# Optimization experiments

Measured on AMD Instinct MI355X. Metric: run time of the kernel, lower is better.

The kernel has to match this reference:

```python
import jax, jax.numpy as jnp
import numpy as np

B, H, S, D = 2, 16, 2048, 64

def setup_inputs() -> dict:
    key = jax.random.key(0)
    kq, kk, kv = jax.random.split(key, 3)
    Q = jax.random.normal(kq, (B, H, S, D), dtype=jnp.float32)
    K = jax.random.normal(kk, (B, H, S, D), dtype=jnp.float32)
    V = jax.random.normal(kv, (B, H, S, D), dtype=jnp.float32)
    return {"Q": Q, "K": K, "V": V}

def reference(Q, K, V):
    # scores: [B, H, S, S]
    scale = 1.0 / jnp.sqrt(jnp.asarray(Q.shape[-1], Q.dtype))
    scores = jnp.einsum('bhqd,bhkd->bhqk', Q, K) * scale
    probs = jax.nn.softmax(scores, axis=-1)
    out = jnp.einsum('bhqk,bhkd->bhqd', probs, V)
    return out
```

## Files before the change

### kernel.cpp

```cpp
#include <hip/hip_runtime.h>
#include <hip/hip_bf16.h>


#define Bn 2
#define Hn 16
#define Sn 2048
#define Dn 64
#define KP 72
#define OP 68

typedef __attribute__((ext_vector_type(8)))  short s16x8;
typedef __attribute__((ext_vector_type(16))) float f32x16;

__device__ __forceinline__ float fast_exp2(float x) {
#if __has_builtin(__builtin_amdgcn_exp2f)
    return __builtin_amdgcn_exp2f(x);
#else
    return exp2f(x);
#endif
}
__device__ __forceinline__ unsigned short f2bf(float f) {
    unsigned u = __float_as_uint(f);
    return (unsigned short)((u + 0x7fffu + ((u >> 16) & 1u)) >> 16);
}
__device__ __forceinline__ unsigned pack2bf(float lo, float hi) {
    return (unsigned)f2bf(lo) | ((unsigned)f2bf(hi) << 16);
}
__device__ __forceinline__ unsigned packtrunc(float lo, float hi) {
#if __has_builtin(__builtin_amdgcn_perm)
    return __builtin_amdgcn_perm(__float_as_uint(hi), __float_as_uint(lo),
                                 0x07060302u);
#else
    return (__float_as_uint(lo) >> 16) | (__float_as_uint(hi) & 0xffff0000u);
#endif
}
__device__ __forceinline__ s16x8 lds_frag(const unsigned short* p) {
    uint4 u = *(const uint4*)p;
    return __builtin_bit_cast(s16x8, u);
}
__device__ __forceinline__ s16x8 reg_frag(uint4 u) {
    return __builtin_bit_cast(s16x8, u);
}

__global__ __launch_bounds__(256)
void cast_kv2(const float* __restrict__ K, const float* __restrict__ V,
              unsigned short* __restrict__ Kb, unsigned short* __restrict__ Vt) {
    __shared__ unsigned short TK[64 * 72];
    __shared__ unsigned short TV[64 * 72];
    const int tid = threadIdx.x;
    const int bh  = blockIdx.x >> 5;
    const int kt  = blockIdx.x & 31;
    const int r = tid >> 2, cc = (tid & 3) * 16;

    const size_t rowbase = ((size_t)bh * Sn + (size_t)kt * 64 + r) * Dn + cc;
    {
        const float* ks = K + rowbase;
        #pragma unroll
        for (int i = 0; i < 2; ++i) {
            float4 f0 = *(const float4*)(ks + 8 * i);
            float4 f1 = *(const float4*)(ks + 8 * i + 4);
            uint4 w;
            w.x = pack2bf(f0.x, f0.y); w.y = pack2bf(f0.z, f0.w);
            w.z = pack2bf(f1.x, f1.y); w.w = pack2bf(f1.z, f1.w);
            *(uint4*)(TK + r * 72 + cc + 8 * i) = w;
        }
    }
    {
        const float* vs = V + rowbase;
        #pragma unroll
        for (int i = 0; i < 4; ++i) {
            float4 f = *(const float4*)(vs + 4 * i);
            const int d0 = cc + 4 * i;
            TV[(d0 + 0) * 72 + r] = f2bf(f.x);
            TV[(d0 + 1) * 72 + r] = f2bf(f.y);
            TV[(d0 + 2) * 72 + r] = f2bf(f.z);
            TV[(d0 + 3) * 72 + r] = f2bf(f.w);
        }
    }
    __syncthreads();
    unsigned short* kd = Kb + ((size_t)(bh * 32 + kt) * 8) * 512;
    unsigned short* vd = Vt + ((size_t)(bh * 32 + kt) * 8) * 512;
    #pragma unroll
    for (int i = 0; i < 2; ++i) {
        const int u = i * 256 + tid;
        const int c = u >> 6, lane = u & 63;
        const int l31 = lane & 31, hf = lane >> 5;
        const int sub = c >> 2, ks = c & 3;
        const int off = (sub * 32 + l31) * 72 + ks * 16 + hf * 8;
        *(uint4*)(kd + c * 512 + lane * 8) = *(const uint4*)(TK + off);
        *(uint4*)(vd + c * 512 + lane * 8) = *(const uint4*)(TV + off);
    }
}

__global__ __launch_bounds__(128, 2)
void attn_fwd_mfma4(const float* __restrict__ Q,
                    const unsigned short* __restrict__ Kb,
                    const unsigned short* __restrict__ Vt,
                    float* __restrict__ O) {
    __shared__ __align__(16) char smem[18432];
    unsigned short* PT = (unsigned short*)smem;
    float* ob = (float*)smem;
    float* lb = ob + 64 * OP;

    const int tid  = threadIdx.x;
    const int wave = tid >> 6;
    const int lane = tid & 63;
    const int l31  = lane & 31;
    const int half = lane >> 5;

    const int bh = blockIdx.x & 31;
    const int q0 = (blockIdx.x >> 5) * 64;

    const float* Qb = Q + ((size_t)bh * Sn + q0) * Dn;
    const float FCT = 0.18033688011112042f;

    s16x8 qf[2][4];
    #pragma unroll
    for (int s = 0; s < 2; ++s) {
        const float* qp = Qb + (size_t)(s * 32 + l31) * Dn;
        #pragma unroll
        for (int ks = 0; ks < 4; ++ks) {
            const int d0 = ks * 16 + half * 8;
            float4 f0 = *(const float4*)(qp + d0);
            float4 f1 = *(const float4*)(qp + d0 + 4);
            uint4 u;
            u.x = pack2bf(f0.x * FCT, f0.y * FCT);
            u.y = pack2bf(f0.z * FCT, f0.w * FCT);
            u.z = pack2bf(f1.x * FCT, f1.y * FCT);
            u.w = pack2bf(f1.z * FCT, f1.w * FCT);
            qf[s][ks] = __builtin_bit_cast(s16x8, u);
        }
    }

    f32x16 acc00, acc01, acc10, acc11;
    #pragma unroll
    for (int r = 0; r < 16; ++r) { acc00[r]=0.f; acc01[r]=0.f; acc10[r]=0.f; acc11[r]=0.f; }
    float l0 = 0.f, l1 = 0.f;

    const unsigned short* kbase =
        Kb + ((size_t)(bh * 32 + wave * 16) * 8) * 512 + (size_t)lane * 8;
    const unsigned short* vbase =
        Vt + ((size_t)(bh * 32 + wave * 16) * 8) * 512 + (size_t)lane * 8;

    unsigned short* ptw0 = PT + ((size_t)wave * 64 + l31) * KP;
    unsigned short* ptw1 = ptw0 + 32 * KP;

    uint4 kbuf[2][8], vv[8];
    #pragma unroll
    for (int c = 0; c < 8; ++c)
        kbuf[0][c] = *(const uint4*)(kbase + c * 512);

    #pragma unroll
    for (int t = 0; t < 16; ++t) {
        uint4* CUR = kbuf[t & 1];
        uint4* NXT = kbuf[(t + 1) & 1];
        #pragma unroll
        for (int c = 0; c < 8; ++c)
            vv[c] = *(const uint4*)(vbase + (size_t)(t * 8 + c) * 512);
        const int tk = (t < 15 ? t + 1 : 15);
        #pragma unroll
        for (int c = 0; c < 8; ++c)
            NXT[c] = *(const uint4*)(kbase + (size_t)(tk * 8 + c) * 512);

        #pragma unroll
        for (int s = 0; s < 2; ++s) {
            f32x16 c0, c1;
            #pragma unroll
            for (int r = 0; r < 16; ++r) { c0[r] = 0.f; c1[r] = 0.f; }
            #pragma unroll
            for (int ks = 0; ks < 4; ++ks) {
                c0 = __builtin_amdgcn_mfma_f32_32x32x16_bf16(reg_frag(CUR[ks]),     qf[s][ks], c0, 0, 0, 0);
                c1 = __builtin_amdgcn_mfma_f32_32x32x16_bf16(reg_frag(CUR[4 + ks]), qf[s][ks], c1, 0, 0, 0);
            }
            #pragma unroll
            for (int r = 0; r < 16; ++r) {
                c0[r] = fast_exp2(c0[r]);
                c1[r] = fast_exp2(c1[r]);
            }
            float a0 = 0.f, a1 = 0.f, a2 = 0.f, a3 = 0.f;
            #pragma unroll
            for (int r = 0; r < 16; r += 4) {
                a0 += c0[r] + c1[r];
                a1 += c0[r + 1] + c1[r + 1];
                a2 += c0[r + 2] + c1[r + 2];
                a3 += c0[r + 3] + c1[r + 3];
            }
            if (s == 0) l0 += (a0 + a1) + (a2 + a3);
            else        l1 += (a0 + a1) + (a2 + a3);

            unsigned short* ptw = s ? ptw1 : ptw0;
            #pragma unroll
            for (int g = 0; g < 4; ++g) {
                uint2 w0, w1;
                w0.x = packtrunc(c0[4 * g + 0], c0[4 * g + 1]);
                w0.y = packtrunc(c0[4 * g + 2], c0[4 * g + 3]);
                w1.x = packtrunc(c1[4 * g + 0], c1[4 * g + 1]);
                w1.y = packtrunc(c1[4 * g + 2], c1[4 * g + 3]);
                *(uint2*)(ptw + 8 * g + 4 * half)      = w0;
                *(uint2*)(ptw + 8 * g + 4 * half + 32) = w1;
            }
        }

        #pragma unroll
        for (int ks = 0; ks < 4; ++ks) {
            const int off = ks * 16 + half * 8;
            s16x8 pf0 = lds_frag(ptw0 + off);
            s16x8 pf1 = lds_frag(ptw1 + off);
            s16x8 va  = reg_frag(vv[ks]);
            s16x8 vb  = reg_frag(vv[4 + ks]);
            acc00 = __builtin_amdgcn_mfma_f32_32x32x16_bf16(va, pf0, acc00, 0, 0, 0);
            acc01 = __builtin_amdgcn_mfma_f32_32x32x16_bf16(vb, pf0, acc01, 0, 0, 0);
            acc10 = __builtin_amdgcn_mfma_f32_32x32x16_bf16(va, pf1, acc10, 0, 0, 0);
            acc11 = __builtin_amdgcn_mfma_f32_32x32x16_bf16(vb, pf1, acc11, 0, 0, 0);
        }
    }

    l0 += __shfl_xor(l0, 32, 64);
    l1 += __shfl_xor(l1, 32, 64);

    __syncthreads();
    if (wave == 0) {
        #pragma unroll
        for (int g = 0; g < 4; ++g) {
            const int d0 = 8 * g + 4 * half;
            float4 f;
            f.x = acc00[4*g+0]; f.y = acc00[4*g+1]; f.z = acc00[4*g+2]; f.w = acc00[4*g+3];
            *(float4*)(ob + l31 * OP + d0) = f;
            f.x = acc01[4*g+0]; f.y = acc01[4*g+1]; f.z = acc01[4*g+2]; f.w = acc01[4*g+3];
            *(float4*)(ob + l31 * OP + d0 + 32) = f;
            f.x = acc10[4*g+0]; f.y = acc10[4*g+1]; f.z = acc10[4*g+2]; f.w = acc10[4*g+3];
            *(float4*)(ob + (32 + l31) * OP + d0) = f;
            f.x = acc11[4*g+0]; f.y = acc11[4*g+1]; f.z = acc11[4*g+2]; f.w = acc11[4*g+3];
            *(float4*)(ob + (32 + l31) * OP + d0 + 32) = f;
        }
        if (half == 0) { lb[l31] = l0; lb[32 + l31] = l1; }
    }
    __syncthreads();
    if (wave == 1) {
        const float i0 = 1.0f / (l0 + lb[l31]);
        const float i1 = 1.0f / (l1 + lb[32 + l31]);
        #pragma unroll
        for (int g = 0; g < 4; ++g) {
            const int d0 = 8 * g + 4 * half;
            float4 f;
            float* p;
            p = ob + l31 * OP + d0;            f = *(float4*)p;
            f.x = (f.x + acc00[4*g+0]) * i0; f.y = (f.y + acc00[4*g+1]) * i0;
            f.z = (f.z + acc00[4*g+2]) * i0; f.w = (f.w + acc00[4*g+3]) * i0;
            *(float4*)p = f;
            p = ob + l31 * OP + d0 + 32;       f = *(float4*)p;
            f.x = (f.x + acc01[4*g+0]) * i0; f.y = (f.y + acc01[4*g+1]) * i0;
            f.z = (f.z + acc01[4*g+2]) * i0; f.w = (f.w + acc01[4*g+3]) * i0;
            *(float4*)p = f;
            p = ob + (32 + l31) * OP + d0;     f = *(float4*)p;
            f.x = (f.x + acc10[4*g+0]) * i1; f.y = (f.y + acc10[4*g+1]) * i1;
            f.z = (f.z + acc10[4*g+2]) * i1; f.w = (f.w + acc10[4*g+3]) * i1;
            *(float4*)p = f;
            p = ob + (32 + l31) * OP + d0 + 32; f = *(float4*)p;
            f.x = (f.x + acc11[4*g+0]) * i1; f.y = (f.y + acc11[4*g+1]) * i1;
            f.z = (f.z + acc11[4*g+2]) * i1; f.w = (f.w + acc11[4*g+3]) * i1;
            *(float4*)p = f;
        }
    }
    __syncthreads();
    float* op = O + ((size_t)bh * Sn + q0) * Dn;
    #pragma unroll
    for (int it = 0; it < 8; ++it) {
        const int idx = it * 128 + tid;
        const int r = idx >> 4, c4 = (idx & 15) * 4;
        *(float4*)(op + r * Dn + c4) = *(float4*)(ob + r * OP + c4);
    }
}

extern "C" void kernel_launch(void* const* d_in, const int* in_sizes, int n_in,
                              void* d_out, int out_size, void* d_ws, size_t ws_size,
                              hipStream_t stream) {
    const float* Q = (const float*)d_in[0];
    const float* K = (const float*)d_in[1];
    const float* V = (const float*)d_in[2];
    float* O = (float*)d_out;

    const size_t elems = (size_t)Bn * Hn * Sn * Dn;
    unsigned short* Kb = (unsigned short*)d_ws;
    unsigned short* Vt = Kb + elems;

    cast_kv2<<<dim3(Bn * Hn * (Sn / 64)), dim3(256), 0, stream>>>(K, V, Kb, Vt);
    attn_fwd_mfma4<<<dim3(Bn * Hn * (Sn / 64)), dim3(128), 0, stream>>>(Q, Kb, Vt, O);
}
```

Measured before the change: 131.5 us.

## Split query rows across four waves per block and drop K double-buffering

The attention kernel now launches 256 threads per block. Each of four waves handles 32 query rows against one half of the keys, where before two waves each handled 64 query rows. This halves per-wave accumulator and register state and doubles the waves available to hide latency. The register double-buffered K prefetch and full unroll of the key-tile loop are removed in favour of a non-unrolled loop with loads issued just before use. Each wave now loads the same K/V tiles as one other wave, so global and L2 traffic per block doubles. Latency hiding now depends on occupancy rather than explicit prefetch.

```diff
diff --git a/kernel.cpp b/kernel.cpp
--- a/kernel.cpp
+++ b/kernel.cpp
@@ -92,8 +92,8 @@
     }
 }
 
-__global__ __launch_bounds__(128, 2)
-void attn_fwd_mfma4(const float* __restrict__ Q,
+__global__ __launch_bounds__(256, 4)
+void attn_fwd_mfma5(const float* __restrict__ Q,
                     const unsigned short* __restrict__ Kb,
                     const unsigned short* __restrict__ Vt,
                     float* __restrict__ O) {
@@ -107,17 +107,17 @@
     const int lane = tid & 63;
     const int l31  = lane & 31;
     const int half = lane >> 5;
+    const int qg   = wave & 1;
+    const int kh   = wave >> 1;
 
     const int bh = blockIdx.x & 31;
     const int q0 = (blockIdx.x >> 5) * 64;
 
-    const float* Qb = Q + ((size_t)bh * Sn + q0) * Dn;
     const float FCT = 0.18033688011112042f;
 
-    s16x8 qf[2][4];
-    #pragma unroll
-    for (int s = 0; s < 2; ++s) {
-        const float* qp = Qb + (size_t)(s * 32 + l31) * Dn;
+    s16x8 qf[4];
+    {
+        const float* qp = Q + ((size_t)bh * Sn + q0 + qg * 32 + l31) * Dn;
         #pragma unroll
         for (int ks = 0; ks < 4; ++ks) {
             const int d0 = ks * 16 + half * 8;
@@ -128,145 +128,116 @@
             u.y = pack2bf(f0.z * FCT, f0.w * FCT);
             u.z = pack2bf(f1.x * FCT, f1.y * FCT);
             u.w = pack2bf(f1.z * FCT, f1.w * FCT);
-            qf[s][ks] = __builtin_bit_cast(s16x8, u);
-        }
-    }
-
-    f32x16 acc00, acc01, acc10, acc11;
+            qf[ks] = __builtin_bit_cast(s16x8, u);
+        }
+    }
+
+    f32x16 acc0, acc1;
     #pragma unroll
-    for (int r = 0; r < 16; ++r) { acc00[r]=0.f; acc01[r]=0.f; acc10[r]=0.f; acc11[r]=0.f; }
-    float l0 = 0.f, l1 = 0.f;
+    for (int r = 0; r < 16; ++r) { acc0[r] = 0.f; acc1[r] = 0.f; }
+    float l = 0.f;
 
     const unsigned short* kbase =
-        Kb + ((size_t)(bh * 32 + wave * 16) * 8) * 512 + (size_t)lane * 8;
+        Kb + ((size_t)(bh * 32 + kh * 16) * 8) * 512 + (size_t)lane * 8;
     const unsigned short* vbase =
-        Vt + ((size_t)(bh * 32 + wave * 16) * 8) * 512 + (size_t)lane * 8;
-
-    unsigned short* ptw0 = PT + ((size_t)wave * 64 + l31) * KP;
-    unsigned short* ptw1 = ptw0 + 32 * KP;
-
-    uint4 kbuf[2][8], vv[8];
-    #pragma unroll
-    for (int c = 0; c < 8; ++c)
-        kbuf[0][c] = *(const uint4*)(kbase + c * 512);
-
-    #pragma unroll
+        Vt + ((size_t)(bh * 32 + kh * 16) * 8) * 512 + (size_t)lane * 8;
+
+    unsigned short* ptw = PT + ((size_t)wave * 32 + l31) * KP;
+
+    #pragma unroll 1
     for (int t = 0; t < 16; ++t) {
-        uint4* CUR = kbuf[t & 1];
-        uint4* NXT = kbuf[(t + 1) & 1];
+        uint4 kk[8];
+        #pragma unroll
+        for (int c = 0; c < 8; ++c)
+            kk[c] = *(const uint4*)(kbase + (size_t)(t * 8 + c) * 512);
+
+        f32x16 c0, c1;
+        #pragma unroll
+        for (int r = 0; r < 16; ++r) { c0[r] = 0.f; c1[r] = 0.f; }
+        #pragma unroll
+        for (int ks = 0; ks < 4; ++ks) {
+            c0 = __builtin_amdgcn_mfma_f32_32x32x16_bf16(reg_frag(kk[ks]),     qf[ks], c0, 0, 0, 0);
+            c1 = __builtin_amdgcn_mfma_f32_32x32x16_bf16(reg_frag(kk[4 + ks]), qf[ks], c1, 0, 0, 0);
+        }
+
+        uint4 vv[8];
         #pragma unroll
         for (int c = 0; c < 8; ++c)
             vv[c] = *(const uint4*)(vbase + (size_t)(t * 8 + c) * 512);
-        const int tk = (t < 15 ? t + 1 : 15);
-        #pragma unroll
-        for (int c = 0; c < 8; ++c)
-            NXT[c] = *(const uint4*)(kbase + (size_t)(tk * 8 + c) * 512);
-
-        #pragma unroll
-        for (int s = 0; s < 2; ++s) {
-            f32x16 c0, c1;
-            #pragma unroll
-            for (int r = 0; r < 16; ++r) { c0[r] = 0.f; c1[r] = 0.f; }
-            #pragma unroll
-            for (int ks = 0; ks < 4; ++ks) {
-                c0 = __builtin_amdgcn_mfma_f32_32x32x16_bf16(reg_frag(CUR[ks]),     qf[s][ks], c0, 0, 0, 0);
-                c1 = __builtin_amdgcn_mfma_f32_32x32x16_bf16(reg_frag(CUR[4 + ks]), qf[s][ks], c1, 0, 0, 0);
-            }
-            #pragma unroll
-            for (int r = 0; r < 16; ++r) {
-                c0[r] = fast_exp2(c0[r]);
-                c1[r] = fast_exp2(c1[r]);
-            }
-            float a0 = 0.f, a1 = 0.f, a2 = 0.f, a3 = 0.f;
-            #pragma unroll
-            for (int r = 0; r < 16; r += 4) {
-                a0 += c0[r] + c1[r];
-                a1 += c0[r + 1] + c1[r + 1];
-                a2 += c0[r + 2] + c1[r + 2];
-                a3 += c0[r + 3] + c1[r + 3];
-            }
-            if (s == 0) l0 += (a0 + a1) + (a2 + a3);
-            else        l1 += (a0 + a1) + (a2 + a3);
-
-            unsigned short* ptw = s ? ptw1 : ptw0;
-            #pragma unroll
-            for (int g = 0; g < 4; ++g) {
-                uint2 w0, w1;
-                w0.x = packtrunc(c0[4 * g + 0], c0[4 * g + 1]);
-                w0.y = packtrunc(c0[4 * g + 2], c0[4 * g + 3]);
-                w1.x = packtrunc(c1[4 * g + 0], c1[4 * g + 1]);
-                w1.y = packtrunc(c1[4 * g + 2], c1[4 * g + 3]);
-                *(uint2*)(ptw + 8 * g + 4 * half)      = w0;
-                *(uint2*)(ptw + 8 * g + 4 * half + 32) = w1;
-            }
+
+        #pragma unroll
+        for (int r = 0; r < 16; ++r) {
+            c0[r] = fast_exp2(c0[r]);
+            c1[r] = fast_exp2(c1[r]);
+        }
+        float a0 = 0.f, a1 = 0.f, a2 = 0.f, a3 = 0.f;
+        #pragma unroll
+        for (int r = 0; r < 16; r += 4) {
+            a0 += c0[r]     + c1[r];
+            a1 += c0[r + 1] + c1[r + 1];
+            a2 += c0[r + 2] + c1[r + 2];
+            a3 += c0[r + 3] + c1[r + 3];
+        }
+        l += (a0 + a1) + (a2 + a3);
+
+        #pragma unroll
+        for (int g = 0; g < 4; ++g) {
+            uint2 w0, w1;
+            w0.x = packtrunc(c0[4 * g + 0], c0[4 * g + 1]);
+            w0.y = packtrunc(c0[4 * g + 2], c0[4 * g + 3]);
+            w1.x = packtrunc(c1[4 * g + 0], c1[4 * g + 1]);
+            w1.y = packtrunc(c1[4 * g + 2], c1[4 * g + 3]);
+            *(uint2*)(ptw + 8 * g + 4 * half)      = w0;
+            *(uint2*)(ptw + 8 * g + 4 * half + 32) = w1;
         }
 
         #pragma unroll
         for (int ks = 0; ks < 4; ++ks) {
-            const int off = ks * 16 + half * 8;
-            s16x8 pf0 = lds_frag(ptw0 + off);
-            s16x8 pf1 = lds_frag(ptw1 + off);
-            s16x8 va  = reg_frag(vv[ks]);
-            s16x8 vb  = reg_frag(vv[4 + ks]);
-            acc00 = __builtin_amdgcn_mfma_f32_32x32x16_bf16(va, pf0, acc00, 0, 0, 0);
-            acc01 = __builtin_amdgcn_mfma_f32_32x32x16_bf16(vb, pf0, acc01, 0, 0, 0);
-            acc10 = __builtin_amdgcn_mfma_f32_32x32x16_bf16(va, pf1, acc10, 0, 0, 0);
-            acc11 = __builtin_amdgcn_mfma_f32_32x32x16_bf16(vb, pf1, acc11, 0, 0, 0);
-        }
-    }
-
-    l0 += __shfl_xor(l0, 32, 64);
-    l1 += __shfl_xor(l1, 32, 64);
-
-    __syncthreads();
-    if (wave == 0) {
+            s16x8 pf = lds_frag(ptw + ks * 16 + half * 8);
+            acc0 = __builtin_amdgcn_mfma_f32_32x32x16_bf16(reg_frag(vv[ks]),     pf, acc0, 0, 0, 0);
+            acc1 = __builtin_amdgcn_mfma_f32_32x32x16_bf16(reg_frag(vv[4 + ks]), pf, acc1, 0, 0, 0);
+        }
+    }
+
+    l += __shfl_xor(l, 32, 64);
+
+    __syncthreads();
+    const int qrow = qg * 32 + l31;
+    if (kh == 0) {
         #pragma unroll
         for (int g = 0; g < 4; ++g) {
             const int d0 = 8 * g + 4 * half;
             float4 f;
-            f.x = acc00[4*g+0]; f.y = acc00[4*g+1]; f.z = acc00[4*g+2]; f.w = acc00[4*g+3];
-            *(float4*)(ob + l31 * OP + d0) = f;
-            f.x = acc01[4*g+0]; f.y = acc01[4*g+1]; f.z = acc01[4*g+2]; f.w = acc01[4*g+3];
-            *(float4*)(ob + l31 * OP + d0 + 32) = f;
-            f.x = acc10[4*g+0]; f.y = acc10[4*g+1]; f.z = acc10[4*g+2]; f.w = acc10[4*g+3];
-            *(float4*)(ob + (32 + l31) * OP + d0) = f;
-            f.x = acc11[4*g+0]; f.y = acc11[4*g+1]; f.z = acc11[4*g+2]; f.w = acc11[4*g+3];
-            *(float4*)(ob + (32 + l31) * OP + d0 + 32) = f;
-        }
-        if (half == 0) { lb[l31] = l0; lb[32 + l31] = l1; }
-    }
-    __syncthreads();
-    if (wave == 1) {
-        const float i0 = 1.0f / (l0 + lb[l31]);
-        const float i1 = 1.0f / (l1 + lb[32 + l31]);
+            f.x = acc0[4*g+0]; f.y = acc0[4*g+1]; f.z = acc0[4*g+2]; f.w = acc0[4*g+3];
+            *(float4*)(ob + qrow * OP + d0) = f;
+            f.x = acc1[4*g+0]; f.y = acc1[4*g+1]; f.z = acc1[4*g+2]; f.w = acc1[4*g+3];
+            *(float4*)(ob + qrow * OP + d0 + 32) = f;
+        }
+        if (half == 0) lb[qrow] = l;
+    }
+    __syncthreads();
+    if (kh == 1) {
+        const float inv = 1.0f / (l + lb[qrow]);
         #pragma unroll
         for (int g = 0; g < 4; ++g) {
             const int d0 = 8 * g + 4 * half;
+            float* p;
             float4 f;
-            float* p;
-            p = ob + l31 * OP + d0;            f = *(float4*)p;
-            f.x = (f.x + acc00[4*g+0]) * i0; f.y = (f.y + acc00[4*g+1]) * i0;
-            f.z = (f.z + acc00[4*g+2]) * i0; f.w = (f.w + acc00[4*g+3]) * i0;
+            p = ob + qrow * OP + d0;        f = *(float4*)p;
+            f.x = (f.x + acc0[4*g+0]) * inv; f.y = (f.y + acc0[4*g+1]) * inv;
+            f.z = (f.z + acc0[4*g+2]) * inv; f.w = (f.w + acc0[4*g+3]) * inv;
             *(float4*)p = f;
-            p = ob + l31 * OP + d0 + 32;       f = *(float4*)p;
-            f.x = (f.x + acc01[4*g+0]) * i0; f.y = (f.y + acc01[4*g+1]) * i0;
-            f.z = (f.z + acc01[4*g+2]) * i0; f.w = (f.w + acc01[4*g+3]) * i0;
-            *(float4*)p = f;
-            p = ob + (32 + l31) * OP + d0;     f = *(float4*)p;
-            f.x = (f.x + acc10[4*g+0]) * i1; f.y = (f.y + acc10[4*g+1]) * i1;
-            f.z = (f.z + acc10[4*g+2]) * i1; f.w = (f.w + acc10[4*g+3]) * i1;
-            *(float4*)p = f;
-            p = ob + (32 + l31) * OP + d0 + 32; f = *(float4*)p;
-            f.x = (f.x + acc11[4*g+0]) * i1; f.y = (f.y + acc11[4*g+1]) * i1;
-            f.z = (f.z + acc11[4*g+2]) * i1; f.w = (f.w + acc11[4*g+3]) * i1;
+            p = ob + qrow * OP + d0 + 32;   f = *(float4*)p;
+            f.x = (f.x + acc1[4*g+0]) * inv; f.y = (f.y + acc1[4*g+1]) * inv;
+            f.z = (f.z + acc1[4*g+2]) * inv; f.w = (f.w + acc1[4*g+3]) * inv;
             *(float4*)p = f;
         }
     }
     __syncthreads();
     float* op = O + ((size_t)bh * Sn + q0) * Dn;
     #pragma unroll
-    for (int it = 0; it < 8; ++it) {
-        const int idx = it * 128 + tid;
+    for (int it = 0; it < 4; ++it) {
+        const int idx = it * 256 + tid;
         const int r = idx >> 4, c4 = (idx & 15) * 4;
         *(float4*)(op + r * Dn + c4) = *(float4*)(ob + r * OP + c4);
     }
@@ -285,5 +256,5 @@
     unsigned short* Vt = Kb + elems;
 
     cast_kv2<<<dim3(Bn * Hn * (Sn / 64)), dim3(256), 0, stream>>>(K, V, Kb, Vt);
-    attn_fwd_mfma4<<<dim3(Bn * Hn * (Sn / 64)), dim3(128), 0, stream>>>(Q, Kb, Vt, O);
-}
+    attn_fwd_mfma5<<<dim3(Bn * Hn * (Sn / 64)), dim3(256), 0, stream>>>(Q, Kb, Vt, O);
+}
```

After: 139.8 us. 6.3% more time.
